# Performance work log

Hardware: AMD Instinct MI355X
Metric: run time of the kernel (lower is better)

The kernel has to match this reference:

```python
import jax, jax.numpy as jnp
import numpy as np

B, C, H, W = 16, 512, 32, 32
EPS = 1e-5

def setup_inputs() -> dict:
    key = jax.random.key(0)
    ks = jax.random.split(key, 7)
    s = 1.0 / np.sqrt(C)
    return {
        "x": jax.random.normal(ks[0], (B, C, H, W), dtype=jnp.float32),
        "norm_w": jnp.ones((C,), jnp.float32),
        "norm_b": jnp.zeros((C,), jnp.float32),
        "qkv_w": jax.random.normal(ks[1], (3 * C, C), dtype=jnp.float32) * s,
        "qkv_b": jax.random.normal(ks[2], (3 * C,), dtype=jnp.float32) * 0.01,
        "out_w": jax.random.normal(ks[3], (C, C), dtype=jnp.float32) * s,
        "out_b": jax.random.normal(ks[4], (C,), dtype=jnp.float32) * 0.01,
    }

def reference(x, norm_w, norm_b, qkv_w, qkv_b, out_w, out_b):
    b, c, h, w = x.shape
    # GroupNorm with num_groups=1: normalize over (C,H,W) per sample, per-channel affine
    mean = jnp.mean(x, axis=(1, 2, 3), keepdims=True)
    var = jnp.var(x, axis=(1, 2, 3), keepdims=True)
    xn = (x - mean) * jax.lax.rsqrt(var + EPS)
    xn = xn * norm_w[None, :, None, None] + norm_b[None, :, None, None]
    # 1x1 conv QKV: [b,3c,h,w]
    qkv = jnp.einsum('bchw,oc->bohw', xn, qkv_w) + qkv_b[None, :, None, None]
    q, k, v = jnp.split(qkv, 3, axis=1)
    n = h * w
    q = q.transpose(0, 2, 3, 1).reshape(b, n, c)   # [b, N, c]
    k = k.reshape(b, c, n)                          # [b, c, N]
    v = v.transpose(0, 2, 3, 1).reshape(b, n, c)   # [b, N, c]
    scores = jnp.einsum('bnc,bcm->bnm', q, k) * (c ** -0.5)  # [b, N, N]
    attn = jax.nn.softmax(scores, axis=-1)
    out = jnp.einsum('bnm,bmc->bnc', attn, v)       # [b, N, c]
    out = out.reshape(b, h, w, c).transpose(0, 3, 1, 2)
    out = jnp.einsum('bchw,oc->bohw', out, out_w) + out_b[None, :, None, None]
    return out + x
```

## Files before the change

### kernel.cpp

```cpp
#include <hip/hip_runtime.h>
#include <math.h>

#define BATCH 16
#define CH    512
#define NTOK  1024
#define CHW   (CH * NTOK)
#define EPSV  1e-5f

typedef __attribute__((ext_vector_type(8))) short bf16x8;
typedef __attribute__((ext_vector_type(4))) float f32x4;

__device__ __forceinline__ unsigned short f2bf(float f) {
    union { float f; unsigned u; } cv; cv.f = f;
    unsigned r = cv.u + 0x7FFFu + ((cv.u >> 16) & 1u);
    return (unsigned short)(r >> 16);
}
__device__ __forceinline__ float bf2f(unsigned short u) {
    union { unsigned u; float f; } cv; cv.u = ((unsigned)u) << 16;
    return cv.f;
}

__device__ __forceinline__ void async16(const unsigned short* g, unsigned short* l) {
    __builtin_amdgcn_global_load_lds(
        (const __attribute__((address_space(1))) void*)g,
        (__attribute__((address_space(3))) void*)l,
        16, 0, 0);
}


static const size_t OFF_WQKV = 256;
static const size_t OFF_OW   = OFF_WQKV + 1572864;
static const size_t OFF_XNT  = OFF_OW   + 524288;
static const size_t OFF_QT   = OFF_XNT  + 16777216;
static const size_t OFF_KT   = OFF_QT   + 16777216;
static const size_t OFF_V    = OFF_KT   + 16777216;
static const size_t OFF_OT   = OFF_V    + 16777216;

__global__ __launch_bounds__(256) void k_stats_partial(const float* __restrict__ x, float* __restrict__ ws) {
    int blk   = blockIdx.x;
    int b     = blk >> 6;
    int chunk = blk & 63;
    const float4* xp = (const float4*)(x + (size_t)b * CHW + (size_t)chunk * 8192);
    int t = threadIdx.x;
    float s = 0.0f, ss = 0.0f;
#pragma unroll
    for (int j = 0; j < 8; j++) {
        float4 v = xp[t + j * 256];
        s  += v.x + v.y + v.z + v.w;
        ss += v.x * v.x + v.y * v.y + v.z * v.z + v.w * v.w;
    }
#pragma unroll
    for (int off = 32; off; off >>= 1) {
        s  += __shfl_xor(s, off, 64);
        ss += __shfl_xor(ss, off, 64);
    }
    __shared__ float ls[4], lss[4];
    int wave = t >> 6, lane = t & 63;
    if (lane == 0) { ls[wave] = s; lss[wave] = ss; }
    __syncthreads();
    if (t == 0) {
        atomicAdd(&ws[b], ls[0] + ls[1] + ls[2] + ls[3]);
        atomicAdd(&ws[16 + b], lss[0] + lss[1] + lss[2] + lss[3]);
    }
}

__global__ void k_stats_final(float* ws) {
    int b = threadIdx.x;
    if (b < 16) {
        float inv  = 1.0f / (float)CHW;
        float mean = ws[b] * inv;
        float var  = ws[16 + b] * inv - mean * mean;
        ws[32 + b] = mean;
        ws[48 + b] = rsqrtf(var + EPSV);
    }
}

__global__ __launch_bounds__(256) void k_cvt2(const float* __restrict__ wq, const float* __restrict__ wo,
                                              unsigned short* __restrict__ WQ, unsigned short* __restrict__ WO,
                                              float* __restrict__ stats) {
    if (blockIdx.x == 0 && threadIdx.x < 64) stats[threadIdx.x] = 0.0f;
    int i = blockIdx.x * 256 + threadIdx.x;
    const float* src; unsigned short* dst; int off;
    if (i < 196608) { src = wq; dst = WQ; off = i; }
    else            { src = wo; dst = WO; off = i - 196608; }
    float4 v = ((const float4*)src)[off];
    ushort4 o;
    o.x = f2bf(v.x); o.y = f2bf(v.y); o.z = f2bf(v.z); o.w = f2bf(v.w);
    ((ushort4*)dst)[off] = o;
}

__global__ __launch_bounds__(256) void k_xnt(const float* __restrict__ x,
                                             const float* __restrict__ nw,
                                             const float* __restrict__ nb,
                                             const float* __restrict__ ws,
                                             unsigned short* __restrict__ xnt) {
    __shared__ float ls[64][65];
    int b  = blockIdx.z;
    int c0 = blockIdx.y * 64;
    int n0 = blockIdx.x * 64;
    float mean = ws[32 + b], rstd = ws[48 + b];
    int t = threadIdx.x;
    int cl = t >> 4, n4 = t & 15;
    const float* xb = x + (size_t)b * CHW;
#pragma unroll
    for (int i = 0; i < 4; i++) {
        int c = c0 + cl + i * 16;
        float a  = rstd * nw[c];
        float bb = nb[c] - mean * a;
        float4 v = *(const float4*)(xb + (size_t)c * NTOK + n0 + n4 * 4);
        ls[cl + i * 16][n4 * 4 + 0] = v.x * a + bb;
        ls[cl + i * 16][n4 * 4 + 1] = v.y * a + bb;
        ls[cl + i * 16][n4 * 4 + 2] = v.z * a + bb;
        ls[cl + i * 16][n4 * 4 + 3] = v.w * a + bb;
    }
    __syncthreads();
    int nl = t >> 4, c4 = t & 15;
    unsigned short* dst = xnt + (size_t)b * NTOK * CH;
#pragma unroll
    for (int i = 0; i < 4; i++) {
        int n = n0 + nl + i * 16;
        ushort4 o;
        o.x = f2bf(ls[c4 * 4 + 0][nl + i * 16]);
        o.y = f2bf(ls[c4 * 4 + 1][nl + i * 16]);
        o.z = f2bf(ls[c4 * 4 + 2][nl + i * 16]);
        o.w = f2bf(ls[c4 * 4 + 3][nl + i * 16]);
        *(ushort4*)(dst + (size_t)n * CH + c0 + c4 * 4) = o;
    }
}

__device__ __forceinline__ void mfma_core2(const unsigned short* __restrict__ A, int lda,
                                           const unsigned short* __restrict__ B, int ldb,
                                           int K, int m0, int n0,
                                           unsigned short* sm,
                                           f32x4 acc[4][8]) {
    const int t = threadIdx.x;
    const int w = t >> 6, lane = t & 63;
    const int wm = (w & 1) * 64, wn = (w >> 1) * 128;
    const int r16 = lane & 15, quad = lane >> 4;
#pragma unroll
    for (int i = 0; i < 4; i++)
#pragma unroll
        for (int j = 0; j < 8; j++) acc[i][j] = (f32x4){0.f, 0.f, 0.f, 0.f};
    const int sr = lane >> 2;
    const int sk = (((lane & 3) ^ ((lane >> 3) & 3))) * 8;
    const int swz = ((quad ^ (r16 >> 1)) & 3) * 8;
    const unsigned short* gA0 = A + (size_t)(m0 + w * 32 + sr) * lda + sk;
    const unsigned short* gA1 = gA0 + (size_t)16 * lda;
    const unsigned short* gB0 = B + (size_t)(n0 + w * 64 + sr) * ldb + sk;
    const unsigned short* gB1 = gB0 + (size_t)16 * ldb;
    const unsigned short* gB2 = gB0 + (size_t)32 * ldb;
    const unsigned short* gB3 = gB0 + (size_t)48 * ldb;
    unsigned short* lA0 = sm + (w * 32) * 32;
    unsigned short* lA1 = sm + (w * 32 + 16) * 32;
    unsigned short* lB0 = sm + 8192 + (w * 64) * 32;
    unsigned short* lB1 = lB0 + 16 * 32;
    unsigned short* lB2 = lB0 + 32 * 32;
    unsigned short* lB3 = lB0 + 48 * 32;
    const int T = K >> 5;
    async16(gA0, lA0); async16(gA1, lA1);
    async16(gB0, lB0); async16(gB1, lB1); async16(gB2, lB2); async16(gB3, lB3);
    for (int tt = 0; tt < T; tt++) {
        __syncthreads();
        const int ab = (tt & 1) << 12;
        const int bb = (tt & 1) << 13;
        if (tt + 1 < T) {
            const int nab = ab ^ 4096, nbb = bb ^ 8192;
            const int ko = (tt + 1) << 5;
            async16(gA0 + ko, lA0 + nab); async16(gA1 + ko, lA1 + nab);
            async16(gB0 + ko, lB0 + nbb); async16(gB1 + ko, lB1 + nbb);
            async16(gB2 + ko, lB2 + nbb); async16(gB3 + ko, lB3 + nbb);
        }
        bf16x8 af[4], bfr[8];
#pragma unroll
        for (int i = 0; i < 4; i++) af[i]  = *(const bf16x8*)(sm + ab + (wm + i * 16 + r16) * 32 + swz);
#pragma unroll
        for (int j = 0; j < 8; j++) bfr[j] = *(const bf16x8*)(sm + 8192 + bb + (wn + j * 16 + r16) * 32 + swz);
#pragma unroll
        for (int i = 0; i < 4; i++)
#pragma unroll
            for (int j = 0; j < 8; j++)
                acc[i][j] = __builtin_amdgcn_mfma_f32_16x16x32_bf16(af[i], bfr[j], acc[i][j], 0, 0, 0);
    }
}

#define TS1 136
#define TS2 264

__global__ __launch_bounds__(256, 2) void k_gemm_qkv(const unsigned short* __restrict__ Wq,
                                                     const float* __restrict__ qb,
                                                     const unsigned short* __restrict__ XNT,
                                                     unsigned short* __restrict__ QT,
                                                     unsigned short* __restrict__ KT,
                                                     unsigned short* __restrict__ V) {
    __shared__ __align__(16) unsigned short smem[256 * TS1];
    const int b  = blockIdx.z;
    const int m0 = blockIdx.y * 128;
    const int n0 = blockIdx.x * 256;
    f32x4 acc[4][8];
    mfma_core2(Wq, CH, XNT + (size_t)b * NTOK * CH, CH, CH, m0, n0, smem, acc);
    const int t = threadIdx.x;
    const int w = t >> 6, lane = t & 63;
    const int wm = (w & 1) * 64, wn = (w >> 1) * 128;
    const int r16 = lane & 15, quad = lane >> 4;
    const int region = m0 >> 9;
    __syncthreads();
    if (region < 2) {
#pragma unroll
        for (int i = 0; i < 4; i++) {
            const int ol = wm + i * 16 + quad * 4;
            const int og = m0 + ol;
            const float b0 = qb[og], b1 = qb[og + 1], b2 = qb[og + 2], b3 = qb[og + 3];
#pragma unroll
            for (int j = 0; j < 8; j++) {
                const int nl = wn + j * 16 + r16;
                f32x4 a = acc[i][j];
                ushort4 pk;
                pk.x = f2bf(a[0] + b0); pk.y = f2bf(a[1] + b1);
                pk.z = f2bf(a[2] + b2); pk.w = f2bf(a[3] + b3);
                *(ushort4*)(smem + nl * TS1 + ol) = pk;
            }
        }
        __syncthreads();
        unsigned short* dst = ((region == 0) ? QT : KT) + (size_t)b * NTOK * CH + (size_t)n0 * CH + (m0 & 511);
#pragma unroll
        for (int p = 0; p < 32; p++) {
            const int row = (t >> 5) + p * 8;
            const int seg = (t & 31) * 4;
            *(ushort4*)(dst + (size_t)row * CH + seg) = *(const ushort4*)(smem + row * TS1 + seg);
        }
    } else {
#pragma unroll
        for (int i = 0; i < 4; i++) {
            const int ol = wm + i * 16 + quad * 4;
            const int og = m0 + ol;
#pragma unroll
            for (int j = 0; j < 8; j++) {
                const int nl = wn + j * 16 + r16;
                f32x4 a = acc[i][j];
#pragma unroll
                for (int r = 0; r < 4; r++)
                    smem[(ol + r) * TS2 + nl] = f2bf(a[r] + qb[og + r]);
            }
        }
        __syncthreads();
        unsigned short* dst = V + (size_t)b * CH * NTOK + (size_t)(m0 & 511) * NTOK + n0;
#pragma unroll
        for (int p = 0; p < 32; p++) {
            const int row = (t >> 5) + (p & 15) * 8;
            const int seg = (t & 31) * 4 + (p >> 4) * 128;
            *(ushort4*)(dst + (size_t)row * NTOK + seg) = *(const ushort4*)(smem + row * TS2 + seg);
        }
    }
}

__global__ __launch_bounds__(512, 2) void k_attn(const unsigned short* __restrict__ QT,
                                                 const unsigned short* __restrict__ KTg,
                                                 const unsigned short* __restrict__ Vg,
                                                 unsigned short* __restrict__ OT) {
    __shared__ __align__(16) unsigned short sm[70400];
    unsigned short* smK = sm;
    unsigned short* smV = sm + 32768;
    unsigned short* smP = sm + 65536;
    float* lsum2 = (float*)(sm + 69888);

    const int bid = blockIdx.x;
    const int xcd = bid & 7, slot = bid >> 3;
    const int b   = xcd * 2 + (slot & 1);
    const int q0  = (slot >> 1) * 64;

    const int t = threadIdx.x;
    const int w = t >> 6, lane = t & 63;
    const int qg = w & 3, h = w >> 2;
    const int r16 = lane & 15, quad = lane >> 4;
    const int srow = lane >> 2;
    const int sc   = (((lane & 3) ^ ((lane >> 3) & 3))) * 8;
    const int swz  = ((quad ^ (r16 >> 1)) & 3) * 8;

    const unsigned short* Qb = QT  + (size_t)b * NTOK * CH;
    const unsigned short* Kb = KTg + (size_t)b * NTOK * CH;
    const unsigned short* Vb = Vg  + (size_t)b * CH * NTOK;

    bf16x8 qf[16];
    {
        const unsigned short* qrow = Qb + (size_t)(q0 + qg * 16 + r16) * CH + quad * 8;
#pragma unroll
        for (int kc = 0; kc < 16; kc++)
            qf[kc] = *(const bf16x8*)(qrow + kc * 32);
    }

    f32x4 accO[16];
#pragma unroll
    for (int j = 0; j < 16; j++) accO[j] = (f32x4){0.f, 0.f, 0.f, 0.f};
    float lsum[4] = {0.f, 0.f, 0.f, 0.f};
    const float scale = 0.044194173824159216f;

#pragma unroll
    for (int kc2 = 0; kc2 < 8; kc2++) {
        const int kc = h * 8 + kc2;
        async16(Kb + (size_t)(qg * 16 + srow) * CH + kc * 32 + sc, smK + (qg * 16 + kc) * 512);
    }
    __syncthreads();

    for (int kt = 0; kt < 16; kt++) {
        {
            const unsigned short* vbase = Vb + (size_t)kt * 64;
#pragma unroll
            for (int cgi = 0; cgi < 4; cgi++) {
                const int cg = w * 4 + cgi;
#pragma unroll
                for (int kk = 0; kk < 2; kk++)
                    async16(vbase + (size_t)(cg * 16 + srow) * NTOK + kk * 32 + sc,
                            smV + (cg * 2 + kk) * 512);
            }
        }
        f32x4 accS[2];
        accS[0] = (f32x4){0.f, 0.f, 0.f, 0.f};
        accS[1] = (f32x4){0.f, 0.f, 0.f, 0.f};
#pragma unroll
        for (int kc = 0; kc < 16; kc++) {
            bf16x8 q = qf[kc];
#pragma unroll
            for (int j = 0; j < 2; j++) {
                const int jj = h * 2 + j;
                bf16x8 kf = *(const bf16x8*)(smK + (jj * 16 + kc) * 512 + r16 * 32 + swz);
                accS[j] = __builtin_amdgcn_mfma_f32_16x16x32_bf16(q, kf, accS[j], 0, 0, 0);
            }
        }
#pragma unroll
        for (int j = 0; j < 2; j++) {
#pragma unroll
            for (int r = 0; r < 4; r++) {
                float e = __expf(accS[j][r] * scale);
                lsum[r] += e;
                smP[(qg * 16 + quad * 4 + r) * 68 + (h * 2 + j) * 16 + r16] = f2bf(e);
            }
        }
        __syncthreads();
        if (kt < 15) {
            const unsigned short* kbase = Kb + (size_t)(kt + 1) * 64 * CH;
#pragma unroll
            for (int kc2 = 0; kc2 < 8; kc2++) {
                const int kc = h * 8 + kc2;
                async16(kbase + (size_t)(qg * 16 + srow) * CH + kc * 32 + sc, smK + (qg * 16 + kc) * 512);
            }
        }
        bf16x8 pf[4][2];
#pragma unroll
        for (int qj = 0; qj < 4; qj++)
#pragma unroll
            for (int kk = 0; kk < 2; kk++)
                pf[qj][kk] = *(const bf16x8*)(smP + (qj * 16 + r16) * 68 + kk * 32 + quad * 8);
#pragma unroll
        for (int cj = 0; cj < 4; cj++) {
            bf16x8 vf0 = *(const bf16x8*)(smV + ((w * 4 + cj) * 2 + 0) * 512 + r16 * 32 + swz);
            bf16x8 vf1 = *(const bf16x8*)(smV + ((w * 4 + cj) * 2 + 1) * 512 + r16 * 32 + swz);
#pragma unroll
            for (int qj = 0; qj < 4; qj++) {
                accO[qj * 4 + cj] = __builtin_amdgcn_mfma_f32_16x16x32_bf16(pf[qj][0], vf0, accO[qj * 4 + cj], 0, 0, 0);
                accO[qj * 4 + cj] = __builtin_amdgcn_mfma_f32_16x16x32_bf16(pf[qj][1], vf1, accO[qj * 4 + cj], 0, 0, 0);
            }
        }
        __syncthreads();
    }

#pragma unroll
    for (int r = 0; r < 4; r++) {
        float v = lsum[r];
        v += __shfl_xor(v, 1, 64);
        v += __shfl_xor(v, 2, 64);
        v += __shfl_xor(v, 4, 64);
        v += __shfl_xor(v, 8, 64);
        if (r16 == 0) lsum2[h * 64 + qg * 16 + quad * 4 + r] = v;
    }
    __syncthreads();
#pragma unroll
    for (int qj = 0; qj < 4; qj++) {
        float iv[4];
#pragma unroll
        for (int r = 0; r < 4; r++) {
            const int row = qj * 16 + quad * 4 + r;
            iv[r] = 1.0f / (lsum2[row] + lsum2[64 + row]);
        }
#pragma unroll
        for (int cj = 0; cj < 4; cj++) {
            f32x4 a = accO[qj * 4 + cj];
#pragma unroll
            for (int r = 0; r < 4; r++)
                sm[(qj * 16 + quad * 4 + r) * 520 + w * 64 + cj * 16 + r16] = f2bf(a[r] * iv[r]);
        }
    }
    __syncthreads();
    unsigned short* dst = OT + (size_t)b * NTOK * CH + (size_t)q0 * CH;
#pragma unroll
    for (int p = 0; p < 16; p++) {
        const int row = (t >> 7) + p * 4;
        const int seg = (t & 127) * 4;
        *(ushort4*)(dst + (size_t)row * CH + seg) = *(const ushort4*)(sm + row * 520 + seg);
    }
}

__global__ __launch_bounds__(256, 2) void k_gemm_out(const unsigned short* __restrict__ OW,
                                                     const float* __restrict__ ob,
                                                     const unsigned short* __restrict__ OT,
                                                     const float* __restrict__ x,
                                                     float* __restrict__ out) {
    __shared__ __align__(16) unsigned short smem[24576];
    const int b  = blockIdx.z;
    const int m0 = blockIdx.y * 128;
    const int n0 = blockIdx.x * 256;
    f32x4 acc[4][8];
    mfma_core2(OW, CH, OT + (size_t)b * NTOK * CH, CH, CH, m0, n0, smem, acc);
    const int t = threadIdx.x;
    const int w = t >> 6, lane = t & 63;
    const int wm = (w & 1) * 64, wn = (w >> 1) * 128;
    const int r16 = lane & 15, quad = lane >> 4;
#pragma unroll
    for (int i = 0; i < 4; i++) {
        const int o0g = m0 + wm + i * 16 + quad * 4;
#pragma unroll
        for (int j = 0; j < 8; j++) {
            const int col = n0 + wn + j * 16 + r16;
            f32x4 a = acc[i][j];
#pragma unroll
            for (int r = 0; r < 4; r++) {
                size_t idx = (size_t)b * CHW + (size_t)(o0g + r) * NTOK + col;
                out[idx] = a[r] + ob[o0g + r] + x[idx];
            }
        }
    }
}

extern "C" void kernel_launch(void* const* d_in, const int* in_sizes, int n_in,
                              void* d_out, int out_size, void* d_ws, size_t ws_size,
                              hipStream_t stream) {
    const float* x      = (const float*)d_in[0];
    const float* norm_w = (const float*)d_in[1];
    const float* norm_b = (const float*)d_in[2];
    const float* qkv_w  = (const float*)d_in[3];
    const float* qkv_b  = (const float*)d_in[4];
    const float* out_w  = (const float*)d_in[5];
    const float* out_b  = (const float*)d_in[6];
    float* out = (float*)d_out;
    char* wsb  = (char*)d_ws;

    float* stats = (float*)wsb;
    unsigned short* WQ  = (unsigned short*)(wsb + OFF_WQKV);
    unsigned short* OW  = (unsigned short*)(wsb + OFF_OW);
    unsigned short* XNT = (unsigned short*)(wsb + OFF_XNT);
    unsigned short* QT  = (unsigned short*)(wsb + OFF_QT);
    unsigned short* KT  = (unsigned short*)(wsb + OFF_KT);
    unsigned short* V   = (unsigned short*)(wsb + OFF_V);
    unsigned short* OT  = (unsigned short*)(wsb + OFF_OT);

    k_cvt2<<<1024, 256, 0, stream>>>(qkv_w, out_w, WQ, OW, stats);
    k_stats_partial<<<BATCH * 64, 256, 0, stream>>>(x, stats);
    k_stats_final<<<1, 16, 0, stream>>>(stats);
    k_xnt<<<dim3(NTOK / 64, CH / 64, BATCH), 256, 0, stream>>>(x, norm_w, norm_b, stats, XNT);
    k_gemm_qkv<<<dim3(NTOK / 256, 3 * CH / 128, BATCH), 256, 0, stream>>>(WQ, qkv_b, XNT, QT, KT, V);
    k_attn<<<256, 512, 0, stream>>>(QT, KT, V, OT);
    k_gemm_out<<<dim3(NTOK / 256, CH / 128, BATCH), 256, 0, stream>>>(OW, out_b, OT, x, out);
}
```

Before: 238.8 us.

## Remap attention QK^T waves to reuse K fragments and fold stats finalize

After: 249.0 us. 1.04x slower.

```diff
diff --git a/kernel.cpp b/kernel.cpp
--- a/kernel.cpp
+++ b/kernel.cpp
@@ -14,10 +14,6 @@
     union { float f; unsigned u; } cv; cv.f = f;
     unsigned r = cv.u + 0x7FFFu + ((cv.u >> 16) & 1u);
     return (unsigned short)(r >> 16);
-}
-__device__ __forceinline__ float bf2f(unsigned short u) {
-    union { unsigned u; float f; } cv; cv.u = ((unsigned)u) << 16;
-    return cv.f;
 }
 
 __device__ __forceinline__ void async16(const unsigned short* g, unsigned short* l) {
@@ -61,17 +57,6 @@
     if (t == 0) {
         atomicAdd(&ws[b], ls[0] + ls[1] + ls[2] + ls[3]);
         atomicAdd(&ws[16 + b], lss[0] + lss[1] + lss[2] + lss[3]);
-    }
-}
-
-__global__ void k_stats_final(float* ws) {
-    int b = threadIdx.x;
-    if (b < 16) {
-        float inv  = 1.0f / (float)CHW;
-        float mean = ws[b] * inv;
-        float var  = ws[16 + b] * inv - mean * mean;
-        ws[32 + b] = mean;
-        ws[48 + b] = rsqrtf(var + EPSV);
     }
 }
 
@@ -98,7 +83,9 @@
     int b  = blockIdx.z;
     int c0 = blockIdx.y * 64;
     int n0 = blockIdx.x * 64;
-    float mean = ws[32 + b], rstd = ws[48 + b];
+    const float inv = 1.0f / (float)CHW;
+    float mean = ws[b] * inv;
+    float rstd = rsqrtf(ws[16 + b] * inv - mean * mean + EPSV);
     int t = threadIdx.x;
     int cl = t >> 4, n4 = t & 15;
     const float* xb = x + (size_t)b * CHW;
@@ -270,7 +257,7 @@
 
     const int t = threadIdx.x;
     const int w = t >> 6, lane = t & 63;
-    const int qg = w & 3, h = w >> 2;
+    const int qg = w & 1, h = w >> 1;
     const int r16 = lane & 15, quad = lane >> 4;
     const int srow = lane >> 2;
     const int sc   = (((lane & 3) ^ ((lane >> 3) & 3))) * 8;
@@ -280,24 +267,27 @@
     const unsigned short* Kb = KTg + (size_t)b * NTOK * CH;
     const unsigned short* Vb = Vg  + (size_t)b * CH * NTOK;
 
-    bf16x8 qf[16];
+    bf16x8 qf[2][16];
     {
-        const unsigned short* qrow = Qb + (size_t)(q0 + qg * 16 + r16) * CH + quad * 8;
-#pragma unroll
-        for (int kc = 0; kc < 16; kc++)
-            qf[kc] = *(const bf16x8*)(qrow + kc * 32);
+        const unsigned short* qrow0 = Qb + (size_t)(q0 + qg * 32 + r16) * CH + quad * 8;
+        const unsigned short* qrow1 = qrow0 + (size_t)16 * CH;
+#pragma unroll
+        for (int kc = 0; kc < 16; kc++) {
+            qf[0][kc] = *(const bf16x8*)(qrow0 + kc * 32);
+            qf[1][kc] = *(const bf16x8*)(qrow1 + kc * 32);
+        }
     }
 
     f32x4 accO[16];
 #pragma unroll
     for (int j = 0; j < 16; j++) accO[j] = (f32x4){0.f, 0.f, 0.f, 0.f};
-    float lsum[4] = {0.f, 0.f, 0.f, 0.f};
+    float lsum[2][4] = {{0.f, 0.f, 0.f, 0.f}, {0.f, 0.f, 0.f, 0.f}};
     const float scale = 0.044194173824159216f;
 
 #pragma unroll
-    for (int kc2 = 0; kc2 < 8; kc2++) {
-        const int kc = h * 8 + kc2;
-        async16(Kb + (size_t)(qg * 16 + srow) * CH + kc * 32 + sc, smK + (qg * 16 + kc) * 512);
+    for (int i = 0; i < 8; i++) {
+        const int ch = w * 8 + i, g = ch >> 4, kc = ch & 15;
+        async16(Kb + (size_t)(g * 16 + srow) * CH + kc * 32 + sc, smK + ch * 512);
     }
     __syncthreads();
 
@@ -318,30 +308,26 @@
         accS[1] = (f32x4){0.f, 0.f, 0.f, 0.f};
 #pragma unroll
         for (int kc = 0; kc < 16; kc++) {
-            bf16x8 q = qf[kc];
-#pragma unroll
-            for (int j = 0; j < 2; j++) {
-                const int jj = h * 2 + j;
-                bf16x8 kf = *(const bf16x8*)(smK + (jj * 16 + kc) * 512 + r16 * 32 + swz);
-                accS[j] = __builtin_amdgcn_mfma_f32_16x16x32_bf16(q, kf, accS[j], 0, 0, 0);
-            }
-        }
-#pragma unroll
-        for (int j = 0; j < 2; j++) {
+            bf16x8 kf = *(const bf16x8*)(smK + (h * 16 + kc) * 512 + r16 * 32 + swz);
+            accS[0] = __builtin_amdgcn_mfma_f32_16x16x32_bf16(qf[0][kc], kf, accS[0], 0, 0, 0);
+            accS[1] = __builtin_amdgcn_mfma_f32_16x16x32_bf16(qf[1][kc], kf, accS[1], 0, 0, 0);
+        }
+#pragma unroll
+        for (int qs = 0; qs < 2; qs++) {
 #pragma unroll
             for (int r = 0; r < 4; r++) {
-                float e = __expf(accS[j][r] * scale);
-                lsum[r] += e;
-                smP[(qg * 16 + quad * 4 + r) * 68 + (h * 2 + j) * 16 + r16] = f2bf(e);
+                float e = __expf(accS[qs][r] * scale);
+                lsum[qs][r] += e;
+                smP[(qg * 32 + qs * 16 + quad * 4 + r) * 68 + h * 16 + r16] = f2bf(e);
             }
         }
         __syncthreads();
         if (kt < 15) {
             const unsigned short* kbase = Kb + (size_t)(kt + 1) * 64 * CH;
 #pragma unroll
-            for (int kc2 = 0; kc2 < 8; kc2++) {
-                const int kc = h * 8 + kc2;
-                async16(kbase + (size_t)(qg * 16 + srow) * CH + kc * 32 + sc, smK + (qg * 16 + kc) * 512);
+            for (int i = 0; i < 8; i++) {
+                const int ch = w * 8 + i, g = ch >> 4, kc = ch & 15;
+                async16(kbase + (size_t)(g * 16 + srow) * CH + kc * 32 + sc, smK + ch * 512);
             }
         }
         bf16x8 pf[4][2];
@@ -364,14 +350,16 @@
     }
 
 #pragma unroll
-    for (int r = 0; r < 4; r++) {
-        float v = lsum[r];
-        v += __shfl_xor(v, 1, 64);
-        v += __shfl_xor(v, 2, 64);
-        v += __shfl_xor(v, 4, 64);
-        v += __shfl_xor(v, 8, 64);
-        if (r16 == 0) lsum2[h * 64 + qg * 16 + quad * 4 + r] = v;
-    }
+    for (int qs = 0; qs < 2; qs++)
+#pragma unroll
+        for (int r = 0; r < 4; r++) {
+            float v = lsum[qs][r];
+            v += __shfl_xor(v, 1, 64);
+            v += __shfl_xor(v, 2, 64);
+            v += __shfl_xor(v, 4, 64);
+            v += __shfl_xor(v, 8, 64);
+            if (r16 == 0) lsum2[h * 64 + qg * 32 + qs * 16 + quad * 4 + r] = v;
+        }
     __syncthreads();
 #pragma unroll
     for (int qj = 0; qj < 4; qj++) {
@@ -379,7 +367,7 @@
 #pragma unroll
         for (int r = 0; r < 4; r++) {
             const int row = qj * 16 + quad * 4 + r;
-            iv[r] = 1.0f / (lsum2[row] + lsum2[64 + row]);
+            iv[r] = 1.0f / (lsum2[row] + lsum2[64 + row] + lsum2[128 + row] + lsum2[192 + row]);
         }
 #pragma unroll
         for (int cj = 0; cj < 4; cj++) {
@@ -454,7 +442,6 @@
 
     k_cvt2<<<1024, 256, 0, stream>>>(qkv_w, out_w, WQ, OW, stats);
     k_stats_partial<<<BATCH * 64, 256, 0, stream>>>(x, stats);
-    k_stats_final<<<1, 16, 0, stream>>>(stats);
     k_xnt<<<dim3(NTOK / 64, CH / 64, BATCH), 256, 0, stream>>>(x, norm_w, norm_b, stats, XNT);
     k_gemm_qkv<<<dim3(NTOK / 256, 3 * CH / 128, BATCH), 256, 0, stream>>>(WQ, qkv_b, XNT, QT, KT, V);
     k_attn<<<256, 512, 0, stream>>>(QT, KT, V, OT);
```
